# Performance work log

Measured on AMD Instinct MI355X. Metric: run time of the kernel, lower is better.

## Reference

```python
import jax, jax.numpy as jnp
import numpy as np

B, T, C = 128, 256, 256
K1, S1, T1 = 2, 2, 128   # conv scale 1: kernel, stride, output time steps
K2, S2, T2 = 4, 4, 64    # conv scale 2
TT = T + T1 + T2         # 448, concatenated time dim fed to TriU
EPS = 1e-5


def hardswish(x):
    return x * jnp.clip(x + 3.0, 0.0, 6.0) / 6.0


def setup_inputs() -> dict:
    key = jax.random.key(0)
    ks = jax.random.split(key, 9)
    return {
        "x": jax.random.normal(ks[0], (B, T, C), jnp.float32),
        "conv_w1": jax.random.normal(ks[1], (C, C, K1), jnp.float32) * 0.05,
        "conv_b1": jax.random.normal(ks[2], (C,), jnp.float32) * 0.05,
        "conv_w2": jax.random.normal(ks[3], (C, C, K2), jnp.float32) * 0.05,
        "conv_b2": jax.random.normal(ks[4], (C,), jnp.float32) * 0.05,
        "ln1_g": jnp.ones((T1, C), jnp.float32),
        "ln1_b": jnp.zeros((T1, C), jnp.float32),
        "ln2_g": jnp.ones((T2, C), jnp.float32),
        "ln2_b": jnp.zeros((T2, C), jnp.float32),
        "triu_w1": jax.random.normal(ks[5], (TT, TT), jnp.float32) * 0.05,
        "triu_b1": jax.random.normal(ks[6], (TT,), jnp.float32) * 0.05,
        "triu_w2": jax.random.normal(ks[7], (TT, TT), jnp.float32) * 0.05,
        "triu_b2": jax.random.normal(ks[8], (TT,), jnp.float32) * 0.05,
    }


def _layernorm2(x, g, b):
    # nn.LayerNorm([ts, C]): normalize jointly over last two dims of [B, ts, C]
    mu = jnp.mean(x, axis=(-2, -1), keepdims=True)
    var = jnp.var(x, axis=(-2, -1), keepdims=True)
    return (x - mu) * jax.lax.rsqrt(var + EPS) * g + b


def _conv1d(x_bct, w, b, stride):
    # x: [B, C, T], w: [Cout, Cin, K] -> [B, Cout, T_out], VALID padding
    y = jax.lax.conv_general_dilated(
        x_bct, w, window_strides=(stride,), padding='VALID',
        dimension_numbers=('NCH', 'OIH', 'NCH'))
    return y + b[None, :, None]


def reference(x, conv_w1, conv_b1, conv_w2, conv_b2,
              ln1_g, ln1_b, ln2_g, ln2_b,
              triu_w1, triu_b1, triu_w2, triu_b2):
    xc = jnp.transpose(x, (0, 2, 1))  # [B, C, T]
    f1 = _layernorm2(jnp.transpose(_conv1d(xc, conv_w1, conv_b1, S1), (0, 2, 1)), ln1_g, ln1_b)
    f2 = _layernorm2(jnp.transpose(_conv1d(xc, conv_w2, conv_b2, S2), (0, 2, 1)), ln2_g, ln2_b)
    cat = jnp.concatenate([x, f1, f2], axis=1)  # [B, TT, C]
    # TriU network on time axis: per-step Linear(i+1,1) == upper-triangular matmul
    z = jnp.transpose(cat, (0, 2, 1))  # [B, C, TT]
    mask = jnp.triu(jnp.ones((TT, TT), z.dtype))  # M[j,i]=w_i[j] for j<=i
    z = hardswish(z @ (triu_w1 * mask) + triu_b1)
    z = z @ (triu_w2 * mask) + triu_b2
    return jnp.transpose(z, (0, 2, 1))  # [B, TT, C]
```

## Files before the change

### kernel.cpp

```cpp
#include <hip/hip_runtime.h>
#include <hip/hip_bf16.h>

#define Bn   128
#define Tn   256
#define Cn   256
#define T1n  128
#define T2n  64
#define TTn  448
#define EPSf 1e-5f

typedef __attribute__((ext_vector_type(8))) short short8;
typedef __attribute__((ext_vector_type(4))) short short4v;
typedef __attribute__((ext_vector_type(4))) float f32x4;

__device__ __forceinline__ unsigned short f2b(float f) {
    union { __hip_bfloat16 h; unsigned short u; } cv;
    cv.h = __float2bfloat16(f);
    return cv.u;
}

__device__ __forceinline__ float b2f(unsigned short u) {
    union { float f; unsigned v; } c;
    c.v = (unsigned)u << 16;
    return c.f;
}

__device__ __forceinline__ short8 cvt8(float4 a, float4 b) {
    short8 r;
    r[0] = (short)f2b(a.x); r[1] = (short)f2b(a.y); r[2] = (short)f2b(a.z); r[3] = (short)f2b(a.w);
    r[4] = (short)f2b(b.x); r[5] = (short)f2b(b.y); r[6] = (short)f2b(b.z); r[7] = (short)f2b(b.w);
    return r;
}

__global__ __launch_bounds__(256) void prep_xpose(
        const float* __restrict__ x,
        const float* __restrict__ cw1, const float* __restrict__ cw2,
        const float* __restrict__ tw1, const float* __restrict__ tw2,
        const float* __restrict__ ln1g, const float* __restrict__ ln1b,
        const float* __restrict__ ln2g, const float* __restrict__ ln2b,
        unsigned short* __restrict__ catb,
        unsigned short* __restrict__ w1rT, unsigned short* __restrict__ w2rT,
        unsigned short* __restrict__ wm1b, unsigned short* __restrict__ wm2b,
        float* __restrict__ gt1, float* __restrict__ bt1,
        float* __restrict__ gt2, float* __restrict__ bt2) {
    __shared__ float tl[64][65];
    const int vb = blockIdx.x;
    if (vb < 2048) {
        int b = vb >> 4, r = vb & 15;
        int t0 = ((r >> 2) & 3) * 64, c0 = (r & 3) * 64;
        const float* xp = x + (size_t)b * Tn * Cn;
        int lr = threadIdx.x >> 4;
        int lc = (threadIdx.x & 15) * 4;
#pragma unroll
        for (int rr = 0; rr < 4; ++rr) {
            int row = lr + rr * 16;
            float4 v = *(const float4*)(xp + (size_t)(t0 + row) * Cn + c0 + lc);
            tl[lc + 0][row] = v.x; tl[lc + 1][row] = v.y;
            tl[lc + 2][row] = v.z; tl[lc + 3][row] = v.w;
        }
        __syncthreads();
        int cr = threadIdx.x >> 2, tq = (threadIdx.x & 3) * 16;
        unsigned short* qp = catb + (size_t)b * (TTn * Cn) + (size_t)(c0 + cr) * TTn + t0 + tq;
        short8 o0, o1;
#pragma unroll
        for (int j = 0; j < 8; ++j) {
            o0[j] = (short)f2b(tl[cr][tq + j]);
            o1[j] = (short)f2b(tl[cr][tq + 8 + j]);
        }
        *(short8*)(qp) = o0;
        *(short8*)(qp + 8) = o1;
        return;
    }
    int idx = (vb - 2048) * 256 + threadIdx.x;
    if (idx < 131072) {
        int co = idx >> 9, r = idx & 511, k = r >> 8, ci = r & 255;
        w1rT[idx] = f2b(cw1[(size_t)co * 512 + ci * 2 + k]);
    } else if ((idx -= 131072) < 262144) {
        int co = idx >> 10, r = idx & 1023, k = r >> 8, ci = r & 255;
        w2rT[idx] = f2b(cw2[(size_t)co * 1024 + ci * 4 + k]);
    } else if ((idx -= 262144) < 200704) {
        int i = idx / TTn, j = idx % TTn;
        wm1b[idx] = (j <= i) ? f2b(tw1[(size_t)j * TTn + i]) : (unsigned short)0;
    } else if ((idx -= 200704) < 200704) {
        int i = idx / TTn, j = idx % TTn;
        wm2b[idx] = (j <= i) ? f2b(tw2[(size_t)j * TTn + i]) : (unsigned short)0;
    } else if ((idx -= 200704) < 32768) {
        int c = idx >> 7, r = idx & 127;
        gt1[idx] = ln1g[(size_t)r * Cn + c];
    } else if ((idx -= 32768) < 32768) {
        int c = idx >> 7, r = idx & 127;
        bt1[idx] = ln1b[(size_t)r * Cn + c];
    } else if ((idx -= 32768) < 16384) {
        int c = idx >> 6, r = idx & 63;
        gt2[idx] = ln2g[(size_t)r * Cn + c];
    } else if ((idx -= 16384) < 16384) {
        int c = idx >> 6, r = idx & 63;
        bt2[idx] = ln2b[(size_t)r * Cn + c];
    }
}

__device__ __forceinline__ void conv_body(char* smem,
        const float* __restrict__ x, int lda,
        const unsigned short* __restrict__ Bw,
        const float* __restrict__ bias,
        unsigned short* __restrict__ Cout, long cstride, int ldc, int K,
        float* __restrict__ psout, int slot, int nslots,
        int m0, int n0, int bz) {
    const int tid = threadIdx.x;
    const int lane = tid & 63;
    const int wid = tid >> 6;
    const int wr = wid >> 1, wc = wid & 1;

    const int ar = tid >> 2, akq = tid & 3;
    const int bn_ = tid >> 1, bkh = (tid & 1) * 32;

    const float* Afp = x + (size_t)bz * (Tn * Cn) + (size_t)(m0 + ar) * lda + akq * 16;
    const unsigned short* Bp = Bw + (size_t)(n0 + bn_) * K + bkh;

    const int awb = ar * 128 + akq * 32;
    const int aswz = (ar & 7) << 4;
    const int bwb = bn_ * 128 + bkh * 2;
    const int bswz = (bn_ & 7) << 4;

    short8 ra0, ra1, rb0, rb1, rb2, rb3;
    auto loadA = [&](int k0) {
        const float* p = Afp + k0;
        float4 v0 = *(const float4*)(p);
        float4 v1 = *(const float4*)(p + 4);
        float4 v2 = *(const float4*)(p + 8);
        float4 v3 = *(const float4*)(p + 12);
        ra0 = cvt8(v0, v1);
        ra1 = cvt8(v2, v3);
    };
    auto loadB = [&](int k0) {
        rb0 = *(const short8*)(Bp + k0);
        rb1 = *(const short8*)(Bp + k0 + 8);
        rb2 = *(const short8*)(Bp + k0 + 16);
        rb3 = *(const short8*)(Bp + k0 + 24);
    };
    auto stage = [&](int buf) {
        char* AsB = smem + buf * 8192;
        char* BsB = smem + 16384 + buf * 16384;
        *(short8*)(AsB + ((awb) ^ aswz)) = ra0;
        *(short8*)(AsB + ((awb + 16) ^ aswz)) = ra1;
        *(short8*)(BsB + ((bwb) ^ bswz)) = rb0;
        *(short8*)(BsB + ((bwb + 16) ^ bswz)) = rb1;
        *(short8*)(BsB + ((bwb + 32) ^ bswz)) = rb2;
        *(short8*)(BsB + ((bwb + 48) ^ bswz)) = rb3;
    };

    const int fl = lane & 15;
    const int fkb = (lane >> 4) * 16;
    const int amb = (wr * 32 + fl) * 128;
    const int bnb = (wc * 64 + fl) * 128;
    const int fswz = (fl & 7) << 4;

    f32x4 acc[2][4];
#pragma unroll
    for (int i = 0; i < 2; ++i)
#pragma unroll
        for (int j = 0; j < 4; ++j) acc[i][j] = (f32x4){0.f, 0.f, 0.f, 0.f};

    const int nkt = K >> 6;
    loadA(0); loadB(0);
    stage(0);
    __syncthreads();
    for (int kt = 0; kt < nkt; ++kt) {
        const int cur = kt & 1;
        if (kt + 1 < nkt) { loadA((kt + 1) * 64); loadB((kt + 1) * 64); }
        char* AsB = smem + cur * 8192;
        char* BsB = smem + 16384 + cur * 16384;
#pragma unroll
        for (int ks = 0; ks < 2; ++ks) {
            const int kb = ks * 64 + fkb;
            short8 af0 = *(const short8*)(AsB + ((amb + kb) ^ fswz));
            short8 af1 = *(const short8*)(AsB + ((amb + 2048 + kb) ^ fswz));
            short8 bf0 = *(const short8*)(BsB + ((bnb + kb) ^ fswz));
            short8 bf1 = *(const short8*)(BsB + ((bnb + 2048 + kb) ^ fswz));
            short8 bf2 = *(const short8*)(BsB + ((bnb + 4096 + kb) ^ fswz));
            short8 bf3 = *(const short8*)(BsB + ((bnb + 6144 + kb) ^ fswz));
            acc[0][0] = __builtin_amdgcn_mfma_f32_16x16x32_bf16(af0, bf0, acc[0][0], 0, 0, 0);
            acc[0][1] = __builtin_amdgcn_mfma_f32_16x16x32_bf16(af0, bf1, acc[0][1], 0, 0, 0);
            acc[0][2] = __builtin_amdgcn_mfma_f32_16x16x32_bf16(af0, bf2, acc[0][2], 0, 0, 0);
            acc[0][3] = __builtin_amdgcn_mfma_f32_16x16x32_bf16(af0, bf3, acc[0][3], 0, 0, 0);
            acc[1][0] = __builtin_amdgcn_mfma_f32_16x16x32_bf16(af1, bf0, acc[1][0], 0, 0, 0);
            acc[1][1] = __builtin_amdgcn_mfma_f32_16x16x32_bf16(af1, bf1, acc[1][1], 0, 0, 0);
            acc[1][2] = __builtin_amdgcn_mfma_f32_16x16x32_bf16(af1, bf2, acc[1][2], 0, 0, 0);
            acc[1][3] = __builtin_amdgcn_mfma_f32_16x16x32_bf16(af1, bf3, acc[1][3], 0, 0, 0);
        }
        if (kt + 1 < nkt) stage(cur ^ 1);
        __syncthreads();
    }

    const int lrow = (lane >> 4) * 4;
    float s_ = 0.f, ss_ = 0.f;
#pragma unroll
    for (int mf = 0; mf < 2; ++mf) {
        const int trow = m0 + wr * 32 + mf * 16 + lrow;
#pragma unroll
        for (int nf = 0; nf < 4; ++nf) {
            const int col = n0 + wc * 64 + nf * 16 + fl;
            f32x4 v = acc[mf][nf];
            v += bias[col];
            short4v pk;
#pragma unroll
            for (int r = 0; r < 4; ++r) {
                s_ += v[r]; ss_ = fmaf(v[r], v[r], ss_);
                pk[r] = (short)f2b(v[r]);
            }
            unsigned short* Cb = Cout + (size_t)bz * cstride + (size_t)col * ldc + trow;
            *(short4v*)Cb = pk;
        }
    }

#pragma unroll
    for (int o = 32; o > 0; o >>= 1) { s_ += __shfl_down(s_, o); ss_ += __shfl_down(ss_, o); }
    float* rsm = (float*)smem;
    if (lane == 0) { rsm[wid] = s_; rsm[wid + 4] = ss_; }
    __syncthreads();
    if (tid == 0) {
        float S = rsm[0] + rsm[1] + rsm[2] + rsm[3];
        float SS = rsm[4] + rsm[5] + rsm[6] + rsm[7];
        psout[((size_t)bz * nslots + slot) * 2 + 0] = S;
        psout[((size_t)bz * nslots + slot) * 2 + 1] = SS;
    }
}

__global__ __launch_bounds__(256) void conv_all(
        const float* __restrict__ x,
        const unsigned short* __restrict__ w1rT, const unsigned short* __restrict__ w2rT,
        const float* __restrict__ cb1, const float* __restrict__ cb2,
        unsigned short* __restrict__ c1t, unsigned short* __restrict__ c2t,
        float* __restrict__ ps1, float* __restrict__ ps2) {
    __shared__ alignas(16) char smem[49152];
    const int y = blockIdx.y, xb = blockIdx.x, bz = blockIdx.z;
    if (y < 2) {
        conv_body(smem, x, 512, w1rT, cb1, c1t, (long)Cn * T1n, T1n, 512,
                  ps1, y * 2 + xb, 4, y * 64, xb * 128, bz);
    } else {
        conv_body(smem, x, 1024, w2rT, cb2, c2t, (long)Cn * T2n, T2n, 1024,
                  ps2, xb, 2, 0, xb * 128, bz);
    }
}

__global__ __launch_bounds__(256) void ln_apply_both(
        const unsigned short* __restrict__ c1t, const unsigned short* __restrict__ c2t,
        const float* __restrict__ gt1, const float* __restrict__ bt1,
        const float* __restrict__ gt2, const float* __restrict__ bt2,
        const float* __restrict__ ps1, const float* __restrict__ ps2,
        unsigned short* __restrict__ catb) {
    const int b = blockIdx.y, bx = blockIdx.x;
    const unsigned short* p;
    const float *g, *be;
    unsigned short* q;
    int LG, n, base;
    float S = 0.f, SS = 0.f;
    if (bx < 16) {
        n = Cn * T1n; LG = 7;
        p = c1t + (size_t)b * n; g = gt1; be = bt1;
        q = catb + (size_t)b * (TTn * Cn) + Tn;
#pragma unroll
        for (int s_ = 0; s_ < 4; ++s_) { S += ps1[b * 8 + s_ * 2]; SS += ps1[b * 8 + s_ * 2 + 1]; }
        base = bx * 2048;
    } else {
        n = Cn * T2n; LG = 6;
        p = c2t + (size_t)b * n; g = gt2; be = bt2;
        q = catb + (size_t)b * (TTn * Cn) + Tn + T1n;
#pragma unroll
        for (int s_ = 0; s_ < 2; ++s_) { S += ps2[b * 4 + s_ * 2]; SS += ps2[b * 4 + s_ * 2 + 1]; }
        base = (bx - 16) * 2048;
    }
    float mu = S / n;
    float rs = rsqrtf(SS / n - mu * mu + EPSf);

    int i = base + threadIdx.x * 8;
    int c = i >> LG, t = i & ((1 << LG) - 1);
    short8 vv = *(const short8*)(p + i);
    float4 g0 = *(const float4*)(g + i);
    float4 g1 = *(const float4*)(g + i + 4);
    float4 b0 = *(const float4*)(be + i);
    float4 b1 = *(const float4*)(be + i + 4);
    float4 o0, o1;
    o0.x = fmaf((b2f((unsigned short)vv[0]) - mu) * rs, g0.x, b0.x);
    o0.y = fmaf((b2f((unsigned short)vv[1]) - mu) * rs, g0.y, b0.y);
    o0.z = fmaf((b2f((unsigned short)vv[2]) - mu) * rs, g0.z, b0.z);
    o0.w = fmaf((b2f((unsigned short)vv[3]) - mu) * rs, g0.w, b0.w);
    o1.x = fmaf((b2f((unsigned short)vv[4]) - mu) * rs, g1.x, b1.x);
    o1.y = fmaf((b2f((unsigned short)vv[5]) - mu) * rs, g1.y, b1.y);
    o1.z = fmaf((b2f((unsigned short)vv[6]) - mu) * rs, g1.z, b1.z);
    o1.w = fmaf((b2f((unsigned short)vv[7]) - mu) * rs, g1.w, b1.w);
    *(short8*)(q + (size_t)c * TTn + t) = cvt8(o0, o1);
}

template<int EPI>
__global__ __launch_bounds__(256)
void triu_db(const unsigned short* __restrict__ Asrc,
             const unsigned short* __restrict__ Bsrc,
             const float* __restrict__ bias,
             void* __restrict__ Cv) {
    const int tid = threadIdx.x;
    const int lane = tid & 63;
    const int wid = tid >> 6;
    const int wr = wid >> 1, wc = wid & 1;

    const int bid = blockIdx.x;
    const int xcd = bid & 7, seq = bid >> 3;
    const int m0 = (seq % 7) * 64;
    const long n0 = (long)(xcd * 32 + seq / 7) * 128;

    __shared__ unsigned short As[2][64 * 64];
    __shared__ unsigned short Bs[2][128 * 64];

    const int ar = tid >> 2, akq = tid & 3;
    const int bn_ = tid >> 1, bkh = (tid & 1) * 32;

    const unsigned short* Ap = Asrc + (size_t)(m0 + ar) * TTn + akq * 16;
    const unsigned short* Bp = Bsrc + (size_t)(n0 + bn_) * TTn + bkh;

    const int awb = ar * 128 + akq * 32;
    const int aswz = (ar & 7) << 4;
    const int bwb = bn_ * 128 + bkh * 2;
    const int bswz = (bn_ & 7) << 4;

    short8 ra0, ra1, rb[4];
    auto loadAB = [&](int k0) {
        ra0 = *(const short8*)(Ap + k0);
        ra1 = *(const short8*)(Ap + k0 + 8);
#pragma unroll
        for (int j = 0; j < 4; ++j) rb[j] = *(const short8*)(Bp + k0 + j * 8);
    };
    auto stage = [&](int buf) {
        char* AsB = (char*)As[buf];
        char* BsB = (char*)Bs[buf];
        *(short8*)(AsB + ((awb) ^ aswz)) = ra0;
        *(short8*)(AsB + ((awb + 16) ^ aswz)) = ra1;
#pragma unroll
        for (int j = 0; j < 4; ++j)
            *(short8*)(BsB + ((bwb + j * 16) ^ bswz)) = rb[j];
    };

    const int fl = lane & 15;
    const int fkb = (lane >> 4) * 16;
    const int amb = (wr * 32 + fl) * 128;
    const int bnb = (wc * 64 + fl) * 128;
    const int fswz = (fl & 7) << 4;

    f32x4 acc[2][4];
#pragma unroll
    for (int i = 0; i < 2; ++i)
#pragma unroll
        for (int j = 0; j < 4; ++j) acc[i][j] = (f32x4){0.f, 0.f, 0.f, 0.f};

    const int nkt = (m0 >> 6) + 1;

    loadAB(0);
    stage(0);
    __syncthreads();
    for (int kt = 0; kt < nkt; ++kt) {
        const int cur = kt & 1;
        if (kt + 1 < nkt) loadAB((kt + 1) * 64);
        char* AsB = (char*)As[cur];
        char* BsB = (char*)Bs[cur];
#pragma unroll
        for (int ks = 0; ks < 2; ++ks) {
            const int kb = ks * 64 + fkb;
            short8 af0 = *(const short8*)(AsB + ((amb + kb) ^ fswz));
            short8 af1 = *(const short8*)(AsB + ((amb + 2048 + kb) ^ fswz));
            short8 bf0 = *(const short8*)(BsB + ((bnb + kb) ^ fswz));
            short8 bf1 = *(const short8*)(BsB + ((bnb + 2048 + kb) ^ fswz));
            short8 bf2 = *(const short8*)(BsB + ((bnb + 4096 + kb) ^ fswz));
            short8 bf3 = *(const short8*)(BsB + ((bnb + 6144 + kb) ^ fswz));
            acc[0][0] = __builtin_amdgcn_mfma_f32_16x16x32_bf16(af0, bf0, acc[0][0], 0, 0, 0);
            acc[0][1] = __builtin_amdgcn_mfma_f32_16x16x32_bf16(af0, bf1, acc[0][1], 0, 0, 0);
            acc[0][2] = __builtin_amdgcn_mfma_f32_16x16x32_bf16(af0, bf2, acc[0][2], 0, 0, 0);
            acc[0][3] = __builtin_amdgcn_mfma_f32_16x16x32_bf16(af0, bf3, acc[0][3], 0, 0, 0);
            acc[1][0] = __builtin_amdgcn_mfma_f32_16x16x32_bf16(af1, bf0, acc[1][0], 0, 0, 0);
            acc[1][1] = __builtin_amdgcn_mfma_f32_16x16x32_bf16(af1, bf1, acc[1][1], 0, 0, 0);
            acc[1][2] = __builtin_amdgcn_mfma_f32_16x16x32_bf16(af1, bf2, acc[1][2], 0, 0, 0);
            acc[1][3] = __builtin_amdgcn_mfma_f32_16x16x32_bf16(af1, bf3, acc[1][3], 0, 0, 0);
        }
        if (kt + 1 < nkt) stage(cur ^ 1);
        __syncthreads();
    }

    const int lrow = (lane >> 4) * 4;
#pragma unroll
    for (int mf = 0; mf < 2; ++mf) {
        const int trow = m0 + wr * 32 + mf * 16 + lrow;
        f32x4 bv = *(const f32x4*)(bias + trow);
#pragma unroll
        for (int nf = 0; nf < 4; ++nf) {
            const long coln = n0 + wc * 64 + nf * 16 + fl;
            f32x4 v = acc[mf][nf] + bv;
            if (EPI == 1) {
                unsigned short* Cb = (unsigned short*)Cv + (size_t)coln * TTn + trow;
                short4v pk;
#pragma unroll
                for (int r = 0; r < 4; ++r) {
                    float t = v[r];
                    float u = fminf(fmaxf(t + 3.f, 0.f), 6.f);
                    t = t * u * (1.f / 6.f);
                    pk[r] = (short)f2b(t);
                }
                *(short4v*)Cb = pk;
            } else {
                const int b = (int)(coln >> 8), c = (int)(coln & 255);
                float* Cb = (float*)Cv + ((size_t)b * TTn + trow) * Cn + c;
#pragma unroll
                for (int r = 0; r < 4; ++r) Cb[(size_t)r * Cn] = v[r];
            }
        }
    }
}

extern "C" void kernel_launch(void* const* d_in, const int* in_sizes, int n_in,
                              void* d_out, int out_size, void* d_ws, size_t ws_size,
                              hipStream_t stream) {
    const float* x    = (const float*)d_in[0];
    const float* cw1  = (const float*)d_in[1];
    const float* cb1  = (const float*)d_in[2];
    const float* cw2  = (const float*)d_in[3];
    const float* cb2  = (const float*)d_in[4];
    const float* ln1g = (const float*)d_in[5];
    const float* ln1b = (const float*)d_in[6];
    const float* ln2g = (const float*)d_in[7];
    const float* ln2b = (const float*)d_in[8];
    const float* tw1  = (const float*)d_in[9];
    const float* tb1  = (const float*)d_in[10];
    const float* tw2  = (const float*)d_in[11];
    const float* tb2  = (const float*)d_in[12];
    float* out = (float*)d_out;

    char* w = (char*)d_ws;
    unsigned short* catb = (unsigned short*)w;
    unsigned short* z1b  = (unsigned short*)(w + 29360128);
    unsigned short* c1t  = (unsigned short*)(w + 58720256);
    unsigned short* c2t  = (unsigned short*)(w + 67108864);
    unsigned short* w1rT = (unsigned short*)(w + 71303168);
    unsigned short* w2rT = (unsigned short*)(w + 71565312);
    unsigned short* wm1b = (unsigned short*)(w + 72089600);
    unsigned short* wm2b = (unsigned short*)(w + 72491008);
    float*          gt1  = (float*)(w + 72892416);
    float*          bt1  = (float*)(w + 73023488);
    float*          gt2  = (float*)(w + 73154560);
    float*          bt2  = (float*)(w + 73220096);
    float*          ps1  = (float*)(w + 73285632);
    float*          ps2  = (float*)(w + 73289728);

    prep_xpose<<<5536, 256, 0, stream>>>(x, cw1, cw2, tw1, tw2, ln1g, ln1b, ln2g, ln2b,
                                         catb, w1rT, w2rT, wm1b, wm2b, gt1, bt1, gt2, bt2);

    conv_all<<<dim3(2, 3, Bn), 256, 0, stream>>>(x, w1rT, w2rT, cb1, cb2, c1t, c2t, ps1, ps2);

    ln_apply_both<<<dim3(24, Bn), 256, 0, stream>>>(c1t, c2t, gt1, bt1, gt2, bt2, ps1, ps2, catb);

    triu_db<1><<<1792, 256, 0, stream>>>(wm1b, catb, tb1, z1b);

    triu_db<2><<<1792, 256, 0, stream>>>(wm2b, z1b, tb2, out);
}
```

Baseline: 93.30 us.

## Load GEMM tiles directly into LDS and schedule longest m-tiles first

```diff
diff --git a/kernel.cpp b/kernel.cpp
--- a/kernel.cpp
+++ b/kernel.cpp
@@ -30,6 +30,12 @@
     r[0] = (short)f2b(a.x); r[1] = (short)f2b(a.y); r[2] = (short)f2b(a.z); r[3] = (short)f2b(a.w);
     r[4] = (short)f2b(b.x); r[5] = (short)f2b(b.y); r[6] = (short)f2b(b.z); r[7] = (short)f2b(b.w);
     return r;
+}
+
+__device__ __forceinline__ void gload_lds16(const void* g, void* l) {
+    __builtin_amdgcn_global_load_lds(
+        (const __attribute__((address_space(1))) unsigned int*)g,
+        (__attribute__((address_space(3))) unsigned int*)l, 16, 0, 0);
 }
 
 __global__ __launch_bounds__(256) void prep_xpose(
@@ -305,38 +311,34 @@
 
     const int bid = blockIdx.x;
     const int xcd = bid & 7, seq = bid >> 3;
-    const int m0 = (seq % 7) * 64;
+    const int mi = 6 - (seq % 7);
+    const int m0 = mi * 64;
     const long n0 = (long)(xcd * 32 + seq / 7) * 128;
 
     __shared__ unsigned short As[2][64 * 64];
     __shared__ unsigned short Bs[2][128 * 64];
 
-    const int ar = tid >> 2, akq = tid & 3;
-    const int bn_ = tid >> 1, bkh = (tid & 1) * 32;
-
-    const unsigned short* Ap = Asrc + (size_t)(m0 + ar) * TTn + akq * 16;
-    const unsigned short* Bp = Bsrc + (size_t)(n0 + bn_) * TTn + bkh;
-
-    const int awb = ar * 128 + akq * 32;
-    const int aswz = (ar & 7) << 4;
-    const int bwb = bn_ * 128 + bkh * 2;
-    const int bswz = (bn_ & 7) << 4;
-
-    short8 ra0, ra1, rb[4];
-    auto loadAB = [&](int k0) {
-        ra0 = *(const short8*)(Ap + k0);
-        ra1 = *(const short8*)(Ap + k0 + 8);
-#pragma unroll
-        for (int j = 0; j < 4; ++j) rb[j] = *(const short8*)(Bp + k0 + j * 8);
-    };
-    auto stage = [&](int buf) {
-        char* AsB = (char*)As[buf];
-        char* BsB = (char*)Bs[buf];
-        *(short8*)(AsB + ((awb) ^ aswz)) = ra0;
-        *(short8*)(AsB + ((awb + 16) ^ aswz)) = ra1;
-#pragma unroll
-        for (int j = 0; j < 4; ++j)
-            *(short8*)(BsB + ((bwb + j * 16) ^ bswz)) = rb[j];
+    const int l8 = lane >> 3, l7 = lane & 7;
+    const int boff = (l7 * 16) ^ ((l8 & 7) << 4);
+    const char* srcb[6];
+#pragma unroll
+    for (int i = 0; i < 6; ++i) {
+        int c = wid * 6 + i;
+        long row = (c < 8) ? (long)(m0 + c * 8 + l8) : (n0 + (long)(c - 8) * 8 + l8);
+        const char* basep = (c < 8) ? (const char*)Asrc : (const char*)Bsrc;
+        srcb[i] = basep + row * (TTn * 2) + boff;
+    }
+    char* a0 = (char*)As[0]; char* a1 = (char*)As[1];
+    char* b0 = (char*)Bs[0]; char* b1 = (char*)Bs[1];
+    auto issue = [&](int buf, int kbyte) {
+        char* ab = buf ? a1 : a0;
+        char* bb = buf ? b1 : b0;
+#pragma unroll
+        for (int i = 0; i < 6; ++i) {
+            int c = wid * 6 + i;
+            char* lp = (c < 8) ? (ab + c * 1024) : (bb + (c - 8) * 1024);
+            gload_lds16(srcb[i] + kbyte, lp);
+        }
     };
 
     const int fl = lane & 15;
@@ -351,16 +353,15 @@
 #pragma unroll
         for (int j = 0; j < 4; ++j) acc[i][j] = (f32x4){0.f, 0.f, 0.f, 0.f};
 
-    const int nkt = (m0 >> 6) + 1;
-
-    loadAB(0);
-    stage(0);
+    const int nkt = mi + 1;
+
+    issue(0, 0);
     __syncthreads();
     for (int kt = 0; kt < nkt; ++kt) {
         const int cur = kt & 1;
-        if (kt + 1 < nkt) loadAB((kt + 1) * 64);
-        char* AsB = (char*)As[cur];
-        char* BsB = (char*)Bs[cur];
+        if (kt + 1 < nkt) issue(cur ^ 1, (kt + 1) * 128);
+        char* AsB = cur ? a1 : a0;
+        char* BsB = cur ? b1 : b0;
 #pragma unroll
         for (int ks = 0; ks < 2; ++ks) {
             const int kb = ks * 64 + fkb;
@@ -379,7 +380,6 @@
             acc[1][2] = __builtin_amdgcn_mfma_f32_16x16x32_bf16(af1, bf2, acc[1][2], 0, 0, 0);
             acc[1][3] = __builtin_amdgcn_mfma_f32_16x16x32_bf16(af1, bf3, acc[1][3], 0, 0, 0);
         }
-        if (kt + 1 < nkt) stage(cur ^ 1);
         __syncthreads();
     }
 
```

Result: no change. 91.60 us (-1.8%).
